# Kernel optimization log

Measured on AMD Instinct MI355X. Metric: run time of the kernel, lower is better.

## Reference

```python
import jax, jax.numpy as jnp
import numpy as np

NUM_HEADS = 4
C_IN = 80   # in_channels[0] (raw camera BEV channels)
C = 126     # in_channels[1]
D = C + 2   # 128, inner attention dim


def _conv(x, w, b=None):
    # NCHW conv, 3x3, SAME padding (padding=1)
    y = jax.lax.conv_general_dilated(x, w, (1, 1), 'SAME',
                                     dimension_numbers=('NCHW', 'OIHW', 'NCHW'))
    if b is not None:
        y = y + b[None, :, None, None]
    return y


def setup_inputs() -> dict:
    key = jax.random.key(0)
    ks = jax.random.split(key, 16)
    s = 0.02
    inp = {
        'lidar_bev': jax.random.normal(ks[0], (1, C, 64, 64), jnp.float32),
        'cam_bev': jax.random.normal(ks[1], (1, C_IN, 64, 64), jnp.float32),
        'cam_enc_w': jax.random.normal(ks[2], (C, C_IN, 3, 3), jnp.float32) * s,
        'cam_enc_b': jnp.zeros((C,), jnp.float32),
        'cam_v_w': jax.random.normal(ks[3], (D, C), jnp.float32) * s,
        'cam_qk_w': jax.random.normal(ks[4], (2 * D, C), jnp.float32) * s,
        'cam_proj_w': jax.random.normal(ks[5], (C, D), jnp.float32) * s,
        'cam_proj_b': jnp.zeros((C,), jnp.float32),
        'lidar_v_w': jax.random.normal(ks[6], (D, C), jnp.float32) * s,
        'lidar_qk_w': jax.random.normal(ks[7], (2 * D, C), jnp.float32) * s,
        'lidar_proj_w': jax.random.normal(ks[8], (C, D), jnp.float32) * s,
        'lidar_proj_b': jnp.zeros((C,), jnp.float32),
        'fuser_w': jax.random.normal(ks[9], (C, 4 * C, 3, 3), jnp.float32) * s,
    }
    return inp


def reference(lidar_bev, cam_bev, cam_enc_w, cam_enc_b, cam_v_w, cam_qk_w,
              cam_proj_w, cam_proj_b, lidar_v_w, lidar_qk_w, lidar_proj_w,
              lidar_proj_b, fuser_w):
    B, Cc, H, W = lidar_bev.shape
    N = H * W
    nh, hd = NUM_HEADS, D // NUM_HEADS
    scale = Cc ** (-0.5)  # in_channels[1] ** -0.5

    cam_enc = _conv(cam_bev, cam_enc_w, cam_enc_b)  # [B,C,H,W] (SCNET stand-in)

    cam_f = cam_enc.reshape(B, Cc, N).transpose(0, 2, 1)     # [B,N,C]
    lid_f = lidar_bev.reshape(B, Cc, N).transpose(0, 2, 1)    # [B,N,C]

    def heads(x):  # [B,N,D] -> [B,nh,N,hd]
        return x.reshape(B, N, nh, hd).transpose(0, 2, 1, 3)

    cam_v = heads(cam_f @ cam_v_w.T)
    lid_v = heads(lid_f @ lidar_v_w.T)

    def qk(x, w):  # -> (q, k) each [B,nh,N,hd]
        t = (x @ w.T).reshape(B, N, 2, nh, hd).transpose(2, 0, 3, 1, 4)
        return t[0], t[1]

    lid_q, lid_k = qk(lid_f, lidar_qk_w)
    cam_q, cam_k = qk(cam_f, cam_qk_w)

    def merge(o):  # [B,nh,N,hd] -> [B,N,D]
        return o.transpose(0, 2, 1, 3).reshape(B, N, D)

    def to_map(x):  # [B,N,C] -> [B,C,H,W]
        return x.reshape(B, H, W, Cc).transpose(0, 3, 1, 2)

    # lidar-driven attention, reused against two value tensors
    lid_attn = jax.nn.softmax(jnp.einsum('bhnd,bhmd->bhnm', lid_q, lid_k) * scale, axis=-1)
    cam_by_lid = to_map(merge(lid_attn @ cam_v) @ cam_proj_w.T + cam_proj_b)
    cam_bev_l = cam_enc + cam_by_lid
    lid_by_lid = to_map(merge(lid_attn @ lid_v) @ lidar_proj_w.T + lidar_proj_b)
    lidar_bev_l = lidar_bev + lid_by_lid

    # camera-driven attention (note: original code uses lidar_proj for BOTH outputs here)
    cam_attn = jax.nn.softmax(jnp.einsum('bhnd,bhmd->bhnm', cam_q, cam_k) * scale, axis=-1)
    cam_by_cam = to_map(merge(cam_attn @ cam_v) @ lidar_proj_w.T + lidar_proj_b)
    cam_bev_c = cam_enc + cam_by_cam
    lid_by_cam = to_map(merge(cam_attn @ lid_v) @ lidar_proj_w.T + lidar_proj_b)
    lidar_bev_c = lidar_bev + lid_by_cam

    fused_in = jnp.concatenate([cam_bev_c, cam_bev_l, lidar_bev_c, lidar_bev_l], axis=1)
    return _conv(fused_in, fuser_w)
```

## Files before the change

### kernel.cpp

```cpp
#include <hip/hip_runtime.h>
#include <hip/hip_bf16.h>

typedef unsigned short ushort_t;
using f32x4  = __attribute__((ext_vector_type(4))) float;
using f32x16 = __attribute__((ext_vector_type(16))) float;
using bf16x8 = __attribute__((ext_vector_type(8))) short;
typedef unsigned uint2v __attribute__((ext_vector_type(2)));

#define N_PIX 4096

static __device__ __forceinline__ unsigned short f2bf(float f) {
  unsigned int u = __builtin_bit_cast(unsigned int, f);
  u += 0x7FFFu + ((u >> 16) & 1u);
  return (unsigned short)(u >> 16);
}
static __device__ __forceinline__ float bf2f(unsigned int us) {
  return __builtin_bit_cast(float, us << 16);
}

typedef union {
  uint4 u4;
  unsigned u[4];
  unsigned long long q[2];
  bf16x8 v;
  unsigned short us[8];
} fragU;

#define LDS_U32(p) ((unsigned)(uintptr_t)((__attribute__((address_space(3))) void*)(p)))

static __device__ __forceinline__ size_t op_off(int s) {
  return (s < 9) ? ((size_t)s << 20)
       : (s == 9)  ? (size_t)15728640u
       : (s == 10) ? (size_t)19456000u
       :             (size_t)21553152u;
}
#define ML_OFF 16777216u

__global__ __launch_bounds__(256) void zero_span_k(uint4* __restrict__ p, int n16) {
  int i = blockIdx.x * 256 + threadIdx.x;
  if (i < n16) p[i] = (uint4){0u, 0u, 0u, 0u};
}

__global__ __launch_bounds__(256) void pack_w_k(
    const float* __restrict__ cam_enc_w, const float* __restrict__ fuser_w,
    const float* __restrict__ lid_proj_w, const float* __restrict__ cam_proj_w,
    const float* __restrict__ lid_qk_w, const float* __restrict__ cam_qk_w,
    const float* __restrict__ cam_v_w, const float* __restrict__ lid_v_w,
    ushort_t* __restrict__ Wp_c, ushort_t* __restrict__ Wp_f,
    ushort_t* __restrict__ Wp_lid, ushort_t* __restrict__ Wp_cam,
    ushort_t* __restrict__ Wq) {
  const float QSCALE = 0.08908708063747479f * 1.4426950408889634f;
  int idx = blockIdx.x * 256 + threadIdx.x;
  if (idx < 110592) {
    int kk = idx / 12288, r = idx % 12288;
    int co = r / 96, ci = r % 96;
    float v = (co < 126 && ci < 80) ? cam_enc_w[(co * 80 + ci) * 9 + kk] : 0.f;
    Wp_c[idx] = f2bf(v);
  } else if (idx < 700416) {
    int j = idx - 110592;
    int kk = j / 65536, r = j % 65536;
    int co = r / 512, ci = r % 512;
    float v = (co < 126 && ci < 504) ? fuser_w[(co * 504 + ci) * 9 + kk] : 0.f;
    Wp_f[j] = f2bf(v);
  } else if (idx < 716800) {
    int j = idx - 700416;
    int co = j >> 7, k = j & 127;
    Wp_lid[j] = f2bf(co < 126 ? lid_proj_w[co * 128 + k] : 0.f);
  } else if (idx < 733184) {
    int j = idx - 716800;
    int co = j >> 7, k = j & 127;
    Wp_cam[j] = f2bf(co < 126 ? cam_proj_w[co * 128 + k] : 0.f);
  } else if (idx < 831488) {
    int j = idx - 733184;
    int t = j >> 14, r = j & 16383;
    int row = r >> 7, ci = r & 127;
    float v = 0.f;
    if (ci < 126) {
      if (t == 0)      v = lid_qk_w[row * 126 + ci] * QSCALE;
      else if (t == 1) v = lid_qk_w[(128 + row) * 126 + ci];
      else if (t == 2) v = cam_qk_w[row * 126 + ci] * QSCALE;
      else if (t == 3) v = cam_qk_w[(128 + row) * 126 + ci];
      else if (t == 4) v = cam_v_w[row * 126 + ci];
      else             v = lid_v_w[row * 126 + ci];
    }
    Wq[j] = f2bf(v);
  }
}

__global__ __launch_bounds__(256) void convert_in_k(
    const float* __restrict__ cam, const float* __restrict__ lidar,
    ushort_t* __restrict__ m, ushort_t* __restrict__ h,
    ushort_t* __restrict__ lidBF) {
  int idx = blockIdx.x * 256 + threadIdx.x;
  if (idx < 327680) {
    int ch = idx >> 12, n = idx & 4095;
    int y = n >> 6, x = n & 63;
    unsigned short b = f2bf(cam[idx]);
    m[ch * 4224 + (y + 1) * 64 + x] = b;
    h[ch * 4356 + (y + 1) * 66 + (x + 1)] = b;
  } else {
    int j = idx - 327680;
    if (j < 516096) lidBF[j] = f2bf(lidar[j]);
  }
}

__global__ __launch_bounds__(256) void conv_mfma_k(
    const ushort_t* __restrict__ Amain,
    const ushort_t* __restrict__ Ahalo,
    const ushort_t* __restrict__ Wp,
    ushort_t* __restrict__ parts,
    int CIp, int ksteps) {
  __shared__ __align__(16) ushort_t Abuf[2][2048];
  const int y   = blockIdx.x;
  const int kk  = blockIdx.y;
  const int ky  = kk / 3, kx = kk - ky * 3;
  const int tid = threadIdx.x;
  const int w   = tid >> 6, l = tid & 63;
  const int lane15 = l & 15, g = l >> 4;
  const int yy1 = y + ky;

  const int ci_l = w * 8 + (l >> 5) * 4 + ((l & 7) >> 1);
  const int m0   = ((l >> 3) & 3) * 16 + (l & 1) * 8;
  const ushort_t* src;
  size_t plane;
  if (kx == 1) { plane = 66 * 64; src = Amain + (size_t)ci_l * plane + yy1 * 64 + m0; }
  else         { plane = 66 * 66; src = Ahalo + (size_t)ci_l * plane + yy1 * 66 + m0 + kx; }

  const ushort_t* wbase = Wp + ((size_t)kk * 128 + w * 32 + lane15) * CIp + g * 8;
  const unsigned tr_base = LDS_U32(&Abuf[0][0]) + (unsigned)(g * 1024 + lane15 * 8);

  f32x4 acc[4][2];
  #pragma unroll
  for (int q = 0; q < 4; ++q) {
    acc[q][0] = (f32x4){0.f, 0.f, 0.f, 0.f};
    acc[q][1] = (f32x4){0.f, 0.f, 0.f, 0.f};
  }

  __builtin_amdgcn_global_load_lds(
      (const __attribute__((address_space(1))) unsigned*)src,
      (__attribute__((address_space(3))) unsigned*)(&Abuf[0][w * 512]), 16, 0, 0);
  __syncthreads();

  for (int s = 0; s < ksteps; ++s) {
    if (s + 1 < ksteps) {
      const ushort_t* srcn = src + (size_t)(s + 1) * 32 * plane;
      __builtin_amdgcn_global_load_lds(
          (const __attribute__((address_space(1))) unsigned*)srcn,
          (__attribute__((address_space(3))) unsigned*)(&Abuf[(s + 1) & 1][w * 512]), 16, 0, 0);
    }
    const ushort_t* wb = wbase + s * 32;
    fragU fb0, fb1;
    fb0.u4 = *(const uint4*)(wb);
    fb1.u4 = *(const uint4*)(wb + 16 * CIp);

    unsigned ta = tr_base + (unsigned)((s & 1) << 12);
    unsigned long long r00, r01, r10, r11, r20, r21, r30, r31;
    asm volatile("ds_read_b64_tr_b16 %0, %1 offset:0"   : "=v"(r00) : "v"(ta));
    asm volatile("ds_read_b64_tr_b16 %0, %1 offset:512" : "=v"(r01) : "v"(ta));
    asm volatile("ds_read_b64_tr_b16 %0, %1 offset:128" : "=v"(r10) : "v"(ta));
    asm volatile("ds_read_b64_tr_b16 %0, %1 offset:640" : "=v"(r11) : "v"(ta));
    asm volatile("ds_read_b64_tr_b16 %0, %1 offset:256" : "=v"(r20) : "v"(ta));
    asm volatile("ds_read_b64_tr_b16 %0, %1 offset:768" : "=v"(r21) : "v"(ta));
    asm volatile("ds_read_b64_tr_b16 %0, %1 offset:384" : "=v"(r30) : "v"(ta));
    asm volatile("ds_read_b64_tr_b16 %0, %1 offset:896" : "=v"(r31) : "v"(ta));
    asm volatile("s_waitcnt lgkmcnt(0)" ::: "memory");
    __builtin_amdgcn_sched_barrier(0);

    fragU fa;
    fa.q[0] = r00; fa.q[1] = r01;
    acc[0][0] = __builtin_amdgcn_mfma_f32_16x16x32_bf16(fa.v, fb0.v, acc[0][0], 0, 0, 0);
    acc[0][1] = __builtin_amdgcn_mfma_f32_16x16x32_bf16(fa.v, fb1.v, acc[0][1], 0, 0, 0);
    fa.q[0] = r10; fa.q[1] = r11;
    acc[1][0] = __builtin_amdgcn_mfma_f32_16x16x32_bf16(fa.v, fb0.v, acc[1][0], 0, 0, 0);
    acc[1][1] = __builtin_amdgcn_mfma_f32_16x16x32_bf16(fa.v, fb1.v, acc[1][1], 0, 0, 0);
    fa.q[0] = r20; fa.q[1] = r21;
    acc[2][0] = __builtin_amdgcn_mfma_f32_16x16x32_bf16(fa.v, fb0.v, acc[2][0], 0, 0, 0);
    acc[2][1] = __builtin_amdgcn_mfma_f32_16x16x32_bf16(fa.v, fb1.v, acc[2][1], 0, 0, 0);
    fa.q[0] = r30; fa.q[1] = r31;
    acc[3][0] = __builtin_amdgcn_mfma_f32_16x16x32_bf16(fa.v, fb0.v, acc[3][0], 0, 0, 0);
    acc[3][1] = __builtin_amdgcn_mfma_f32_16x16x32_bf16(fa.v, fb1.v, acc[3][1], 0, 0, 0);
    __syncthreads();
  }

  ushort_t* pout = parts + (size_t)kk * 524288 + (size_t)(w * 32 + lane15) * 4096
                 + y * 64 + g * 4;
  #pragma unroll
  for (int q = 0; q < 4; ++q) {
    ushort4 p0, p1;
    p0.x = f2bf(acc[q][0][0]); p0.y = f2bf(acc[q][0][1]);
    p0.z = f2bf(acc[q][0][2]); p0.w = f2bf(acc[q][0][3]);
    p1.x = f2bf(acc[q][1][0]); p1.y = f2bf(acc[q][1][1]);
    p1.z = f2bf(acc[q][1][2]); p1.w = f2bf(acc[q][1][3]);
    *(ushort4*)(pout + q * 16)             = p0;
    *(ushort4*)(pout + 16 * 4096 + q * 16) = p1;
  }
}

__global__ __launch_bounds__(256) void reduce9_k(
    const ushort_t* __restrict__ parts, float* __restrict__ out,
    ushort_t* __restrict__ outbf, const float* __restrict__ bias) {
  int n0 = (blockIdx.x * 256 + threadIdx.x) * 8;
  int co = blockIdx.y;
  size_t off = (size_t)co * 4096 + n0;
  float s[8] = {0, 0, 0, 0, 0, 0, 0, 0};
  #pragma unroll
  for (int kk = 0; kk < 9; ++kk) {
    uint4 v = *(const uint4*)(parts + (size_t)kk * 524288 + off);
    s[0] += bf2f(v.x & 0xffffu); s[1] += bf2f(v.x >> 16);
    s[2] += bf2f(v.y & 0xffffu); s[3] += bf2f(v.y >> 16);
    s[4] += bf2f(v.z & 0xffffu); s[5] += bf2f(v.z >> 16);
    s[6] += bf2f(v.w & 0xffffu); s[7] += bf2f(v.w >> 16);
  }
  float b = bias ? bias[co] : 0.f;
  #pragma unroll
  for (int i = 0; i < 8; ++i) s[i] += b;
  if (out) {
    f32x4 o0 = {s[0], s[1], s[2], s[3]};
    f32x4 o1 = {s[4], s[5], s[6], s[7]};
    *(f32x4*)(out + off)     = o0;
    *(f32x4*)(out + off + 4) = o1;
  }
  if (outbf) {
    ushort4 b0, b1;
    b0.x = f2bf(s[0]); b0.y = f2bf(s[1]); b0.z = f2bf(s[2]); b0.w = f2bf(s[3]);
    b1.x = f2bf(s[4]); b1.y = f2bf(s[5]); b1.z = f2bf(s[6]); b1.w = f2bf(s[7]);
    *(ushort4*)(outbf + off)     = b0;
    *(ushort4*)(outbf + off + 4) = b1;
  }
}

__global__ __launch_bounds__(256) void qkv_mfma_k(
    const ushort_t* __restrict__ lidBF, const ushort_t* __restrict__ camBF,
    const ushort_t* __restrict__ Wq,
    ushort_t* __restrict__ lidQK, ushort_t* __restrict__ camQK,
    ushort_t* __restrict__ camV, ushort_t* __restrict__ lidV) {
  __shared__ __align__(16) ushort_t Abuf[2][2048];
  const int y = blockIdx.x, t = blockIdx.y;
  const ushort_t* X = (t >= 2 && t <= 4) ? camBF : lidBF;
  const int tid = threadIdx.x;
  const int w = tid >> 6, l = tid & 63;
  const int lane15 = l & 15, g = l >> 4;
  const int ci_l = w * 8 + (l >> 5) * 4 + ((l & 7) >> 1);
  const int m0   = ((l >> 3) & 3) * 16 + (l & 1) * 8;
  const ushort_t* src = X + (size_t)ci_l * 4096 + y * 64 + m0;
  const ushort_t* wbase = Wq + (size_t)t * 16384 + (w * 32 + lane15) * 128 + g * 8;
  const unsigned tr_base = LDS_U32(&Abuf[0][0]) + (unsigned)(g * 1024 + lane15 * 8);

  f32x4 acc[4][2];
  #pragma unroll
  for (int q = 0; q < 4; ++q) {
    acc[q][0] = (f32x4){0.f, 0.f, 0.f, 0.f};
    acc[q][1] = (f32x4){0.f, 0.f, 0.f, 0.f};
  }

  __builtin_amdgcn_global_load_lds(
      (const __attribute__((address_space(1))) unsigned*)src,
      (__attribute__((address_space(3))) unsigned*)(&Abuf[0][w * 512]), 16, 0, 0);
  __syncthreads();

  for (int s = 0; s < 4; ++s) {
    if (s < 3) {
      const ushort_t* srcn = src + (size_t)(s + 1) * 32 * 4096;
      __builtin_amdgcn_global_load_lds(
          (const __attribute__((address_space(1))) unsigned*)srcn,
          (__attribute__((address_space(3))) unsigned*)(&Abuf[(s + 1) & 1][w * 512]), 16, 0, 0);
    }
    const ushort_t* wb = wbase + s * 32;
    fragU fb0, fb1;
    fb0.u4 = *(const uint4*)(wb);
    fb1.u4 = *(const uint4*)(wb + 16 * 128);

    unsigned ta = tr_base + (unsigned)((s & 1) << 12);
    unsigned long long r00, r01, r10, r11, r20, r21, r30, r31;
    asm volatile("ds_read_b64_tr_b16 %0, %1 offset:0"   : "=v"(r00) : "v"(ta));
    asm volatile("ds_read_b64_tr_b16 %0, %1 offset:512" : "=v"(r01) : "v"(ta));
    asm volatile("ds_read_b64_tr_b16 %0, %1 offset:128" : "=v"(r10) : "v"(ta));
    asm volatile("ds_read_b64_tr_b16 %0, %1 offset:640" : "=v"(r11) : "v"(ta));
    asm volatile("ds_read_b64_tr_b16 %0, %1 offset:256" : "=v"(r20) : "v"(ta));
    asm volatile("ds_read_b64_tr_b16 %0, %1 offset:768" : "=v"(r21) : "v"(ta));
    asm volatile("ds_read_b64_tr_b16 %0, %1 offset:384" : "=v"(r30) : "v"(ta));
    asm volatile("ds_read_b64_tr_b16 %0, %1 offset:896" : "=v"(r31) : "v"(ta));
    asm volatile("s_waitcnt lgkmcnt(0)" ::: "memory");
    __builtin_amdgcn_sched_barrier(0);

    fragU fa;
    fa.q[0] = r00; fa.q[1] = r01;
    acc[0][0] = __builtin_amdgcn_mfma_f32_16x16x32_bf16(fa.v, fb0.v, acc[0][0], 0, 0, 0);
    acc[0][1] = __builtin_amdgcn_mfma_f32_16x16x32_bf16(fa.v, fb1.v, acc[0][1], 0, 0, 0);
    fa.q[0] = r10; fa.q[1] = r11;
    acc[1][0] = __builtin_amdgcn_mfma_f32_16x16x32_bf16(fa.v, fb0.v, acc[1][0], 0, 0, 0);
    acc[1][1] = __builtin_amdgcn_mfma_f32_16x16x32_bf16(fa.v, fb1.v, acc[1][1], 0, 0, 0);
    fa.q[0] = r20; fa.q[1] = r21;
    acc[2][0] = __builtin_amdgcn_mfma_f32_16x16x32_bf16(fa.v, fb0.v, acc[2][0], 0, 0, 0);
    acc[2][1] = __builtin_amdgcn_mfma_f32_16x16x32_bf16(fa.v, fb1.v, acc[2][1], 0, 0, 0);
    fa.q[0] = r30; fa.q[1] = r31;
    acc[3][0] = __builtin_amdgcn_mfma_f32_16x16x32_bf16(fa.v, fb0.v, acc[3][0], 0, 0, 0);
    acc[3][1] = __builtin_amdgcn_mfma_f32_16x16x32_bf16(fa.v, fb1.v, acc[3][1], 0, 0, 0);
    __syncthreads();
  }

  if (t < 4) {
    ushort_t* dst = (t < 2) ? lidQK : camQK;
    const int colbase = (t & 1) * 128 + w * 32 + lane15;
    #pragma unroll
    for (int q = 0; q < 4; ++q)
      #pragma unroll
      for (int tt = 0; tt < 2; ++tt)
        #pragma unroll
        for (int r = 0; r < 4; ++r) {
          int n = y * 64 + q * 16 + g * 4 + r;
          dst[(size_t)n * 256 + colbase + tt * 16] = f2bf(acc[q][tt][r]);
        }
  } else {
    ushort_t* dst = (t == 4) ? camV : lidV;
    ushort_t* pout = dst + (size_t)(w * 32 + lane15) * 4096 + y * 64 + g * 4;
    #pragma unroll
    for (int q = 0; q < 4; ++q) {
      ushort4 p0, p1;
      p0.x = f2bf(acc[q][0][0]); p0.y = f2bf(acc[q][0][1]);
      p0.z = f2bf(acc[q][0][2]); p0.w = f2bf(acc[q][0][3]);
      p1.x = f2bf(acc[q][1][0]); p1.y = f2bf(acc[q][1][1]);
      p1.z = f2bf(acc[q][1][2]); p1.w = f2bf(acc[q][1][3]);
      *(ushort4*)(pout + q * 16)             = p0;
      *(ushort4*)(pout + 16 * 4096 + q * 16) = p1;
    }
  }
}

__global__ __launch_bounds__(256) void flash_attn_mfma(
    const ushort_t* __restrict__ lidQK, const ushort_t* __restrict__ camQK,
    const ushort_t* __restrict__ camV, const ushort_t* __restrict__ lidV,
    char* __restrict__ ws) {
  const int i0    = blockIdx.x * 128;
  const int h     = blockIdx.y;
  const int z     = blockIdx.z;
  const int attn  = (z >= 3) ? 1 : 0;
  const int third = z - attn * 3;
  const int kbase = (third == 0) ? 0 : (1408 + (third - 1) * 1344);
  const int iters = (third == 0) ? 22 : 21;
  const ushort_t* QK = attn ? camQK : lidQK;

  __shared__ __align__(16) ushort_t Ks[2][64 * 40];
  __shared__ __align__(16) ushort_t Vt[2][64 * 72];

  const int tid = threadIdx.x;
  const int w = tid >> 6, l = tid & 63;
  const int q31 = l & 31, hi = l >> 5;
  const int q0w = i0 + w * 32;

  const int srow = tid >> 2, sc = tid & 3;
  const ushort_t* Kg = QK + (size_t)(kbase + srow) * 256 + 128 + h * 32 + sc * 8;
  const ushort_t* Vg = ((srow >> 5) ? lidV : camV)
                     + (size_t)(h * 32 + (srow & 31)) * N_PIX + kbase;

  fragU qf0, qf1;
  qf0.u4 = *(const uint4*)(QK + (size_t)(q0w + q31) * 256 + h * 32 + hi * 8);
  qf1.u4 = *(const uint4*)(QK + (size_t)(q0w + q31) * 256 + h * 32 + 16 + hi * 8);

  {
    uint4 k4 = *(const uint4*)Kg;
    uint4 va = *(const uint4*)(Vg + sc * 8);
    uint4 vb = *(const uint4*)(Vg + (sc + 4) * 8);
    *(uint4*)(&Ks[0][srow * 40 + sc * 8]) = k4;
    *(uint4*)(&Vt[0][srow * 72 + sc * 8]) = va;
    *(uint4*)(&Vt[0][srow * 72 + (sc + 4) * 8]) = vb;
  }
  __syncthreads();

  f32x16 Oc = (f32x16)0.f, Ol = (f32x16)0.f;
  float lrun = 0.f, mrun = -1e30f;

  for (int it = 0; it < iters; ++it) {
    const int cur = it & 1, nxt = cur ^ 1;
    const bool more = (it + 1) < iters;
    uint4 kn, van, vbn;
    if (more) {
      kn  = *(const uint4*)(Kg + (size_t)(it + 1) * 16384);
      van = *(const uint4*)(Vg + (it + 1) * 64 + sc * 8);
      vbn = *(const uint4*)(Vg + (it + 1) * 64 + (sc + 4) * 8);
    }

    const ushort_t* kb = &Ks[cur][0];
    fragU k00, k01, k10, k11;
    k00.u4 = *(const uint4*)(kb + q31 * 40 + hi * 8);
    k01.u4 = *(const uint4*)(kb + q31 * 40 + 16 + hi * 8);
    k10.u4 = *(const uint4*)(kb + (32 + q31) * 40 + hi * 8);
    k11.u4 = *(const uint4*)(kb + (32 + q31) * 40 + 16 + hi * 8);
    f32x16 S0, S1;
    __builtin_amdgcn_s_setprio(1);
    S0 = __builtin_amdgcn_mfma_f32_32x32x16_bf16(k00.v, qf0.v, (f32x16)0.f, 0, 0, 0);
    S0 = __builtin_amdgcn_mfma_f32_32x32x16_bf16(k01.v, qf1.v, S0, 0, 0, 0);
    S1 = __builtin_amdgcn_mfma_f32_32x32x16_bf16(k10.v, qf0.v, (f32x16)0.f, 0, 0, 0);
    S1 = __builtin_amdgcn_mfma_f32_32x32x16_bf16(k11.v, qf1.v, S1, 0, 0, 0);
    __builtin_amdgcn_s_setprio(0);

    float mx = S0[0];
    #pragma unroll
    for (int j = 1; j < 16; ++j) mx = fmaxf(mx, S0[j]);
    #pragma unroll
    for (int j = 0; j < 16; ++j) mx = fmaxf(mx, S1[j]);
    if (__any(mx > mrun + 6.f)) {
      float gm = mx;
      gm = fmaxf(gm, __shfl_xor(gm, 1));
      gm = fmaxf(gm, __shfl_xor(gm, 2));
      gm = fmaxf(gm, __shfl_xor(gm, 4));
      gm = fmaxf(gm, __shfl_xor(gm, 8));
      gm = fmaxf(gm, __shfl_xor(gm, 16));
      gm = fmaxf(gm, __shfl_xor(gm, 32));
      if (gm > mrun) {
        float corr = __builtin_amdgcn_exp2f(mrun - gm);
        Oc = Oc * corr;
        Ol = Ol * corr;
        lrun *= corr;
        mrun = gm;
      }
    }
    float ps = 0.f;
    #pragma unroll
    for (int j = 0; j < 16; ++j) {
      float p = __builtin_amdgcn_exp2f(S0[j] - mrun);
      S0[j] = p; ps += p;
    }
    #pragma unroll
    for (int j = 0; j < 16; ++j) {
      float p = __builtin_amdgcn_exp2f(S1[j] - mrun);
      S1[j] = p; ps += p;
    }
    ps += __shfl_xor(ps, 32);
    lrun += ps;

    fragU pa0, pa1, pa2, pa3;
    {
      unsigned a0, a1, b0, b1;
      asm("v_cvt_pk_bf16_f32 %0, %1, %2" : "=v"(a0) : "v"(S0[0]),  "v"(S0[1]));
      asm("v_cvt_pk_bf16_f32 %0, %1, %2" : "=v"(a1) : "v"(S0[2]),  "v"(S0[3]));
      asm("v_cvt_pk_bf16_f32 %0, %1, %2" : "=v"(b0) : "v"(S0[4]),  "v"(S0[5]));
      asm("v_cvt_pk_bf16_f32 %0, %1, %2" : "=v"(b1) : "v"(S0[6]),  "v"(S0[7]));
      uint2v r0 = __builtin_amdgcn_permlane32_swap(a0, b0, false, false);
      uint2v r1 = __builtin_amdgcn_permlane32_swap(a1, b1, false, false);
      pa0.u[0] = r0[0]; pa0.u[1] = r1[0]; pa0.u[2] = r0[1]; pa0.u[3] = r1[1];
      asm("v_cvt_pk_bf16_f32 %0, %1, %2" : "=v"(a0) : "v"(S0[8]),  "v"(S0[9]));
      asm("v_cvt_pk_bf16_f32 %0, %1, %2" : "=v"(a1) : "v"(S0[10]), "v"(S0[11]));
      asm("v_cvt_pk_bf16_f32 %0, %1, %2" : "=v"(b0) : "v"(S0[12]), "v"(S0[13]));
      asm("v_cvt_pk_bf16_f32 %0, %1, %2" : "=v"(b1) : "v"(S0[14]), "v"(S0[15]));
      r0 = __builtin_amdgcn_permlane32_swap(a0, b0, false, false);
      r1 = __builtin_amdgcn_permlane32_swap(a1, b1, false, false);
      pa1.u[0] = r0[0]; pa1.u[1] = r1[0]; pa1.u[2] = r0[1]; pa1.u[3] = r1[1];
      asm("v_cvt_pk_bf16_f32 %0, %1, %2" : "=v"(a0) : "v"(S1[0]),  "v"(S1[1]));
      asm("v_cvt_pk_bf16_f32 %0, %1, %2" : "=v"(a1) : "v"(S1[2]),  "v"(S1[3]));
      asm("v_cvt_pk_bf16_f32 %0, %1, %2" : "=v"(b0) : "v"(S1[4]),  "v"(S1[5]));
      asm("v_cvt_pk_bf16_f32 %0, %1, %2" : "=v"(b1) : "v"(S1[6]),  "v"(S1[7]));
      r0 = __builtin_amdgcn_permlane32_swap(a0, b0, false, false);
      r1 = __builtin_amdgcn_permlane32_swap(a1, b1, false, false);
      pa2.u[0] = r0[0]; pa2.u[1] = r1[0]; pa2.u[2] = r0[1]; pa2.u[3] = r1[1];
      asm("v_cvt_pk_bf16_f32 %0, %1, %2" : "=v"(a0) : "v"(S1[8]),  "v"(S1[9]));
      asm("v_cvt_pk_bf16_f32 %0, %1, %2" : "=v"(a1) : "v"(S1[10]), "v"(S1[11]));
      asm("v_cvt_pk_bf16_f32 %0, %1, %2" : "=v"(b0) : "v"(S1[12]), "v"(S1[13]));
      asm("v_cvt_pk_bf16_f32 %0, %1, %2" : "=v"(b1) : "v"(S1[14]), "v"(S1[15]));
      r0 = __builtin_amdgcn_permlane32_swap(a0, b0, false, false);
      r1 = __builtin_amdgcn_permlane32_swap(a1, b1, false, false);
      pa3.u[0] = r0[0]; pa3.u[1] = r1[0]; pa3.u[2] = r0[1]; pa3.u[3] = r1[1];
    }

    const ushort_t* vb = &Vt[cur][0];
    __builtin_amdgcn_s_setprio(1);
    {
      fragU vc, vl;
      vc.u4 = *(const uint4*)(vb + q31 * 72 + hi * 8);
      vl.u4 = *(const uint4*)(vb + (32 + q31) * 72 + hi * 8);
      Oc = __builtin_amdgcn_mfma_f32_32x32x16_bf16(pa0.v, vc.v, Oc, 0, 0, 0);
      Ol = __builtin_amdgcn_mfma_f32_32x32x16_bf16(pa0.v, vl.v, Ol, 0, 0, 0);
      vc.u4 = *(const uint4*)(vb + q31 * 72 + 16 + hi * 8);
      vl.u4 = *(const uint4*)(vb + (32 + q31) * 72 + 16 + hi * 8);
      Oc = __builtin_amdgcn_mfma_f32_32x32x16_bf16(pa1.v, vc.v, Oc, 0, 0, 0);
      Ol = __builtin_amdgcn_mfma_f32_32x32x16_bf16(pa1.v, vl.v, Ol, 0, 0, 0);
      vc.u4 = *(const uint4*)(vb + q31 * 72 + 32 + hi * 8);
      vl.u4 = *(const uint4*)(vb + (32 + q31) * 72 + 32 + hi * 8);
      Oc = __builtin_amdgcn_mfma_f32_32x32x16_bf16(pa2.v, vc.v, Oc, 0, 0, 0);
      Ol = __builtin_amdgcn_mfma_f32_32x32x16_bf16(pa2.v, vl.v, Ol, 0, 0, 0);
      vc.u4 = *(const uint4*)(vb + q31 * 72 + 48 + hi * 8);
      vl.u4 = *(const uint4*)(vb + (32 + q31) * 72 + 48 + hi * 8);
      Oc = __builtin_amdgcn_mfma_f32_32x32x16_bf16(pa3.v, vc.v, Oc, 0, 0, 0);
      Ol = __builtin_amdgcn_mfma_f32_32x32x16_bf16(pa3.v, vl.v, Ol, 0, 0, 0);
    }
    __builtin_amdgcn_s_setprio(0);

    if (more) {
      *(uint4*)(&Ks[nxt][srow * 40 + sc * 8]) = kn;
      *(uint4*)(&Vt[nxt][srow * 72 + sc * 8]) = van;
      *(uint4*)(&Vt[nxt][srow * 72 + (sc + 4) * 8]) = vbn;
    }
    __syncthreads();
  }

  const int si = (attn * 3 + third) * 2;
  ushort_t* OPc = (ushort_t*)(ws + op_off(si + 0));
  ushort_t* OPl = (ushort_t*)(ws + op_off(si + 1));
  float2* ML = (float2*)(ws + ML_OFF);
  const int d = h * 32 + q31;
  #pragma unroll
  for (int reg = 0; reg < 16; ++reg) {
    int n = q0w + (reg & 3) + 8 * (reg >> 2) + 4 * hi;
    OPc[(size_t)n * 128 + d] = f2bf(Oc[reg]);
    OPl[(size_t)n * 128 + d] = f2bf(Ol[reg]);
  }
  if (l < 32) {
    float2 v; v.x = mrun; v.y = lrun;
    ML[(size_t)(attn * 3 + third) * 4096 + q0w + l] = v;
  }
}

__global__ __launch_bounds__(256) void proj_mfma_k(
    const char* __restrict__ ws,
    const ushort_t* __restrict__ Wlid, const ushort_t* __restrict__ Wcam,
    const ushort_t* __restrict__ camBF, const float* __restrict__ lidar_bev,
    const float* __restrict__ cam_proj_b, const float* __restrict__ lid_proj_b,
    ushort_t* __restrict__ fm, ushort_t* __restrict__ fh) {
  const int n0 = blockIdx.x * 64;
  const int ot = blockIdx.y;
  const int attn = (ot == 0 || ot == 2) ? 1 : 0;
  const int vt = ot >> 1;
  const int tid = threadIdx.x;
  const int w = tid >> 6, l = tid & 63;
  const int m = l & 15, g = l >> 4;

  const float2* ML = (const float2*)(ws + ML_OFF);
  const int arow = n0 + w * 16 + m;

  float2 ml0 = ML[(size_t)(attn * 3 + 0) * 4096 + arow];
  float2 ml1 = ML[(size_t)(attn * 3 + 1) * 4096 + arow];
  float2 ml2 = ML[(size_t)(attn * 3 + 2) * 4096 + arow];
  float M = fmaxf(fmaxf(ml0.x, ml1.x), ml2.x);
  float w0 = __builtin_amdgcn_exp2f(ml0.x - M);
  float w1 = __builtin_amdgcn_exp2f(ml1.x - M);
  float w2 = __builtin_amdgcn_exp2f(ml2.x - M);
  float dn = w0 * ml0.y + w1 * ml1.y + w2 * ml2.y;
  float a0 = w0 / dn, a1 = w1 / dn, a2 = w2 / dn;

  const ushort_t* O0 = (const ushort_t*)(ws + op_off((attn * 3 + 0) * 2 + vt));
  const ushort_t* O1 = (const ushort_t*)(ws + op_off((attn * 3 + 1) * 2 + vt));
  const ushort_t* O2 = (const ushort_t*)(ws + op_off((attn * 3 + 2) * 2 + vt));

  fragU afr[4];
  #pragma unroll
  for (int s = 0; s < 4; ++s) {
    fragU x0, x1, x2;
    x0.u4 = *(const uint4*)(O0 + (size_t)arow * 128 + s * 32 + g * 8);
    x1.u4 = *(const uint4*)(O1 + (size_t)arow * 128 + s * 32 + g * 8);
    x2.u4 = *(const uint4*)(O2 + (size_t)arow * 128 + s * 32 + g * 8);
    #pragma unroll
    for (int j = 0; j < 8; ++j)
      afr[s].us[j] = f2bf(a0 * bf2f(x0.us[j]) + a1 * bf2f(x1.us[j])
                        + a2 * bf2f(x2.us[j]));
  }

  const ushort_t* W = (ot == 1) ? Wcam : Wlid;
  f32x4 acc[8];
  #pragma unroll
  for (int t = 0; t < 8; ++t) acc[t] = (f32x4){0.f, 0.f, 0.f, 0.f};
  #pragma unroll
  for (int s = 0; s < 4; ++s) {
    #pragma unroll
    for (int t = 0; t < 8; ++t) {
      fragU bfr;
      bfr.u4 = *(const uint4*)(W + (size_t)(t * 16 + m) * 128 + s * 32 + g * 8);
      acc[t] = __builtin_amdgcn_mfma_f32_16x16x32_bf16(afr[s].v, bfr.v, acc[t], 0, 0, 0);
    }
  }

  const float* bias = (ot == 1) ? cam_proj_b : lid_proj_b;
  const int doff = ot * 126;
  #pragma unroll
  for (int t = 0; t < 8; ++t) {
    int co = t * 16 + m;
    if (co < 126) {
      float b = bias[co];
      #pragma unroll
      for (int r = 0; r < 4; ++r) {
        int n = n0 + w * 16 + g * 4 + r;
        float res = (ot < 2) ? bf2f(camBF[(size_t)co * N_PIX + n])
                             : lidar_bev[(size_t)co * N_PIX + n];
        float v = acc[t][r] + res + b;
        unsigned short bf = f2bf(v);
        int y = n >> 6, x = n & 63;
        fm[(doff + co) * 4224 + (y + 1) * 64 + x]      = bf;
        fh[(doff + co) * 4356 + (y + 1) * 66 + x + 1]  = bf;
      }
    }
  }
}

extern "C" void kernel_launch(void* const* d_in, const int* in_sizes, int n_in,
                              void* d_out, int out_size, void* d_ws, size_t ws_size,
                              hipStream_t stream) {
  (void)in_sizes; (void)n_in; (void)out_size; (void)ws_size;
  const float* lidar_bev  = (const float*)d_in[0];
  const float* cam_bev    = (const float*)d_in[1];
  const float* cam_enc_w  = (const float*)d_in[2];
  const float* cam_enc_b  = (const float*)d_in[3];
  const float* cam_v_w    = (const float*)d_in[4];
  const float* cam_qk_w   = (const float*)d_in[5];
  const float* cam_proj_w = (const float*)d_in[6];
  const float* cam_proj_b = (const float*)d_in[7];
  const float* lid_v_w    = (const float*)d_in[8];
  const float* lid_qk_w   = (const float*)d_in[9];
  const float* lid_proj_w = (const float*)d_in[10];
  const float* lid_proj_b = (const float*)d_in[11];
  const float* fuser_w    = (const float*)d_in[12];
  float* out = (float*)d_out;

  char* p = (char*)d_ws;
  ushort_t* arena = (ushort_t*)p;
  ushort_t* lidQK = (ushort_t*)(p + 9437184);
  ushort_t* camQK = (ushort_t*)(p + 11534336);
  ushort_t* camV  = (ushort_t*)(p + 13631488);
  ushort_t* lidV  = (ushort_t*)(p + 14680064);
  ushort_t* Wp_c    = (ushort_t*)(p + 17793024);
  ushort_t* Wp_f    = (ushort_t*)(p + 18014208);
  ushort_t* Wp_lid  = (ushort_t*)(p + 19193856);
  ushort_t* Wp_cam  = (ushort_t*)(p + 19226624);
  ushort_t* Wq      = (ushort_t*)(p + 19259392);
  ushort_t* lidBF   = (ushort_t*)(p + 19456000);
  ushort_t* camBF   = (ushort_t*)(p + 20504576);
  ushort_t* camBF_m = (ushort_t*)(p + 21553152);
  ushort_t* camBF_h = (ushort_t*)(p + 22364160);
  ushort_t* fusBF_m = (ushort_t*)(p + 23200512);
  ushort_t* fusBF_h = (ushort_t*)(p + 27525888);

  zero_span_k<<<2548, 256, 0, stream>>>((uint4*)(p + 21553152), 652080);
  pack_w_k<<<3248, 256, 0, stream>>>(cam_enc_w, fuser_w, lid_proj_w, cam_proj_w,
                                     lid_qk_w, cam_qk_w, cam_v_w, lid_v_w,
                                     Wp_c, Wp_f, Wp_lid, Wp_cam, Wq);
  convert_in_k<<<3296, 256, 0, stream>>>(cam_bev, lidar_bev, camBF_m, camBF_h, lidBF);

  conv_mfma_k<<<dim3(64, 9), 256, 0, stream>>>(camBF_m, camBF_h, Wp_c, arena, 96, 3);
  reduce9_k<<<dim3(2, 126), 256, 0, stream>>>(arena, nullptr, camBF, cam_enc_b);

  qkv_mfma_k<<<dim3(64, 6), 256, 0, stream>>>(lidBF, camBF, Wq, lidQK, camQK, camV, lidV);
  flash_attn_mfma<<<dim3(32, 4, 6), 256, 0, stream>>>(lidQK, camQK, camV, lidV, p);
  proj_mfma_k<<<dim3(64, 4), 256, 0, stream>>>(p, Wp_lid, Wp_cam, camBF, lidar_bev,
                                               cam_proj_b, lid_proj_b, fusBF_m, fusBF_h);

  conv_mfma_k<<<dim3(64, 9), 256, 0, stream>>>(fusBF_m, fusBF_h, Wp_f, arena, 512, 16);
  reduce9_k<<<dim3(2, 126), 256, 0, stream>>>(arena, out, nullptr, nullptr);
}
```

Measured before the change: 119.8 us.

## Load flash-attention K/V fragments directly from global and merge prep kernels

The flash attention kernel drops its double-buffered LDS staging of K and V tiles and the per-iteration block barrier. Each wave now loads its MFMA operand fragments straight from global memory (relying on L2/L1 for reuse across the four waves). Separately, the weight-packing and input-conversion kernels are merged into one launch to save a kernel launch. The risk is redundant global traffic and exposed load latency without the software prefetch.

```diff
diff --git a/kernel.cpp b/kernel.cpp
--- a/kernel.cpp
+++ b/kernel.cpp
@@ -41,14 +41,17 @@
   if (i < n16) p[i] = (uint4){0u, 0u, 0u, 0u};
 }
 
-__global__ __launch_bounds__(256) void pack_w_k(
+__global__ __launch_bounds__(256) void prep_k(
     const float* __restrict__ cam_enc_w, const float* __restrict__ fuser_w,
     const float* __restrict__ lid_proj_w, const float* __restrict__ cam_proj_w,
     const float* __restrict__ lid_qk_w, const float* __restrict__ cam_qk_w,
     const float* __restrict__ cam_v_w, const float* __restrict__ lid_v_w,
+    const float* __restrict__ cam_bev, const float* __restrict__ lidar_bev,
     ushort_t* __restrict__ Wp_c, ushort_t* __restrict__ Wp_f,
     ushort_t* __restrict__ Wp_lid, ushort_t* __restrict__ Wp_cam,
-    ushort_t* __restrict__ Wq) {
+    ushort_t* __restrict__ Wq,
+    ushort_t* __restrict__ cm, ushort_t* __restrict__ ch_,
+    ushort_t* __restrict__ lidBF) {
   const float QSCALE = 0.08908708063747479f * 1.4426950408889634f;
   int idx = blockIdx.x * 256 + threadIdx.x;
   if (idx < 110592) {
@@ -84,23 +87,18 @@
       else             v = lid_v_w[row * 126 + ci];
     }
     Wq[j] = f2bf(v);
-  }
-}
-
-__global__ __launch_bounds__(256) void convert_in_k(
-    const float* __restrict__ cam, const float* __restrict__ lidar,
-    ushort_t* __restrict__ m, ushort_t* __restrict__ h,
-    ushort_t* __restrict__ lidBF) {
-  int idx = blockIdx.x * 256 + threadIdx.x;
-  if (idx < 327680) {
-    int ch = idx >> 12, n = idx & 4095;
-    int y = n >> 6, x = n & 63;
-    unsigned short b = f2bf(cam[idx]);
-    m[ch * 4224 + (y + 1) * 64 + x] = b;
-    h[ch * 4356 + (y + 1) * 66 + (x + 1)] = b;
   } else {
-    int j = idx - 327680;
-    if (j < 516096) lidBF[j] = f2bf(lidar[j]);
+    int k = idx - 831488;
+    if (k < 327680) {
+      int ch = k >> 12, n = k & 4095;
+      int y = n >> 6, x = n & 63;
+      unsigned short b = f2bf(cam_bev[k]);
+      cm[ch * 4224 + (y + 1) * 64 + x] = b;
+      ch_[ch * 4356 + (y + 1) * 66 + (x + 1)] = b;
+    } else {
+      int j = k - 327680;
+      if (j < 516096) lidBF[j] = f2bf(lidar_bev[j]);
+    }
   }
 }
 
@@ -340,52 +338,41 @@
   const int iters = (third == 0) ? 22 : 21;
   const ushort_t* QK = attn ? camQK : lidQK;
 
-  __shared__ __align__(16) ushort_t Ks[2][64 * 40];
-  __shared__ __align__(16) ushort_t Vt[2][64 * 72];
-
   const int tid = threadIdx.x;
   const int w = tid >> 6, l = tid & 63;
   const int q31 = l & 31, hi = l >> 5;
   const int q0w = i0 + w * 32;
 
-  const int srow = tid >> 2, sc = tid & 3;
-  const ushort_t* Kg = QK + (size_t)(kbase + srow) * 256 + 128 + h * 32 + sc * 8;
-  const ushort_t* Vg = ((srow >> 5) ? lidV : camV)
-                     + (size_t)(h * 32 + (srow & 31)) * N_PIX + kbase;
-
   fragU qf0, qf1;
   qf0.u4 = *(const uint4*)(QK + (size_t)(q0w + q31) * 256 + h * 32 + hi * 8);
   qf1.u4 = *(const uint4*)(QK + (size_t)(q0w + q31) * 256 + h * 32 + 16 + hi * 8);
 
-  {
-    uint4 k4 = *(const uint4*)Kg;
-    uint4 va = *(const uint4*)(Vg + sc * 8);
-    uint4 vb = *(const uint4*)(Vg + (sc + 4) * 8);
-    *(uint4*)(&Ks[0][srow * 40 + sc * 8]) = k4;
-    *(uint4*)(&Vt[0][srow * 72 + sc * 8]) = va;
-    *(uint4*)(&Vt[0][srow * 72 + (sc + 4) * 8]) = vb;
-  }
-  __syncthreads();
+  const ushort_t* Kp = QK + (size_t)(kbase + q31) * 256 + 128 + h * 32 + hi * 8;
+  const ushort_t* Vc = camV + (size_t)(h * 32 + q31) * N_PIX + kbase + hi * 8;
+  const ushort_t* Vl = lidV + (size_t)(h * 32 + q31) * N_PIX + kbase + hi * 8;
 
   f32x16 Oc = (f32x16)0.f, Ol = (f32x16)0.f;
   float lrun = 0.f, mrun = -1e30f;
 
   for (int it = 0; it < iters; ++it) {
-    const int cur = it & 1, nxt = cur ^ 1;
-    const bool more = (it + 1) < iters;
-    uint4 kn, van, vbn;
-    if (more) {
-      kn  = *(const uint4*)(Kg + (size_t)(it + 1) * 16384);
-      van = *(const uint4*)(Vg + (it + 1) * 64 + sc * 8);
-      vbn = *(const uint4*)(Vg + (it + 1) * 64 + (sc + 4) * 8);
-    }
-
-    const ushort_t* kb = &Ks[cur][0];
     fragU k00, k01, k10, k11;
-    k00.u4 = *(const uint4*)(kb + q31 * 40 + hi * 8);
-    k01.u4 = *(const uint4*)(kb + q31 * 40 + 16 + hi * 8);
-    k10.u4 = *(const uint4*)(kb + (32 + q31) * 40 + hi * 8);
-    k11.u4 = *(const uint4*)(kb + (32 + q31) * 40 + 16 + hi * 8);
+    const ushort_t* kp = Kp + (size_t)it * 16384;
+    k00.u4 = *(const uint4*)(kp);
+    k01.u4 = *(const uint4*)(kp + 16);
+    k10.u4 = *(const uint4*)(kp + 8192);
+    k11.u4 = *(const uint4*)(kp + 8192 + 16);
+    fragU vc0, vc1, vc2, vc3, vl0, vl1, vl2, vl3;
+    const ushort_t* vcp = Vc + it * 64;
+    const ushort_t* vlp = Vl + it * 64;
+    vc0.u4 = *(const uint4*)(vcp);
+    vc1.u4 = *(const uint4*)(vcp + 16);
+    vc2.u4 = *(const uint4*)(vcp + 32);
+    vc3.u4 = *(const uint4*)(vcp + 48);
+    vl0.u4 = *(const uint4*)(vlp);
+    vl1.u4 = *(const uint4*)(vlp + 16);
+    vl2.u4 = *(const uint4*)(vlp + 32);
+    vl3.u4 = *(const uint4*)(vlp + 48);
+
     f32x16 S0, S1;
     __builtin_amdgcn_s_setprio(1);
     S0 = __builtin_amdgcn_mfma_f32_32x32x16_bf16(k00.v, qf0.v, (f32x16)0.f, 0, 0, 0);
@@ -462,35 +449,16 @@
       pa3.u[0] = r0[0]; pa3.u[1] = r1[0]; pa3.u[2] = r0[1]; pa3.u[3] = r1[1];
     }
 
-    const ushort_t* vb = &Vt[cur][0];
     __builtin_amdgcn_s_setprio(1);
-    {
-      fragU vc, vl;
-      vc.u4 = *(const uint4*)(vb + q31 * 72 + hi * 8);
-      vl.u4 = *(const uint4*)(vb + (32 + q31) * 72 + hi * 8);
-      Oc = __builtin_amdgcn_mfma_f32_32x32x16_bf16(pa0.v, vc.v, Oc, 0, 0, 0);
-      Ol = __builtin_amdgcn_mfma_f32_32x32x16_bf16(pa0.v, vl.v, Ol, 0, 0, 0);
-      vc.u4 = *(const uint4*)(vb + q31 * 72 + 16 + hi * 8);
-      vl.u4 = *(const uint4*)(vb + (32 + q31) * 72 + 16 + hi * 8);
-      Oc = __builtin_amdgcn_mfma_f32_32x32x16_bf16(pa1.v, vc.v, Oc, 0, 0, 0);
-      Ol = __builtin_amdgcn_mfma_f32_32x32x16_bf16(pa1.v, vl.v, Ol, 0, 0, 0);
-      vc.u4 = *(const uint4*)(vb + q31 * 72 + 32 + hi * 8);
-      vl.u4 = *(const uint4*)(vb + (32 + q31) * 72 + 32 + hi * 8);
-      Oc = __builtin_amdgcn_mfma_f32_32x32x16_bf16(pa2.v, vc.v, Oc, 0, 0, 0);
-      Ol = __builtin_amdgcn_mfma_f32_32x32x16_bf16(pa2.v, vl.v, Ol, 0, 0, 0);
-      vc.u4 = *(const uint4*)(vb + q31 * 72 + 48 + hi * 8);
-      vl.u4 = *(const uint4*)(vb + (32 + q31) * 72 + 48 + hi * 8);
-      Oc = __builtin_amdgcn_mfma_f32_32x32x16_bf16(pa3.v, vc.v, Oc, 0, 0, 0);
-      Ol = __builtin_amdgcn_mfma_f32_32x32x16_bf16(pa3.v, vl.v, Ol, 0, 0, 0);
-    }
+    Oc = __builtin_amdgcn_mfma_f32_32x32x16_bf16(pa0.v, vc0.v, Oc, 0, 0, 0);
+    Ol = __builtin_amdgcn_mfma_f32_32x32x16_bf16(pa0.v, vl0.v, Ol, 0, 0, 0);
+    Oc = __builtin_amdgcn_mfma_f32_32x32x16_bf16(pa1.v, vc1.v, Oc, 0, 0, 0);
+    Ol = __builtin_amdgcn_mfma_f32_32x32x16_bf16(pa1.v, vl1.v, Ol, 0, 0, 0);
+    Oc = __builtin_amdgcn_mfma_f32_32x32x16_bf16(pa2.v, vc2.v, Oc, 0, 0, 0);
+    Ol = __builtin_amdgcn_mfma_f32_32x32x16_bf16(pa2.v, vl2.v, Ol, 0, 0, 0);
+    Oc = __builtin_amdgcn_mfma_f32_32x32x16_bf16(pa3.v, vc3.v, Oc, 0, 0, 0);
+    Ol = __builtin_amdgcn_mfma_f32_32x32x16_bf16(pa3.v, vl3.v, Ol, 0, 0, 0);
     __builtin_amdgcn_s_setprio(0);
-
-    if (more) {
-      *(uint4*)(&Ks[nxt][srow * 40 + sc * 8]) = kn;
-      *(uint4*)(&Vt[nxt][srow * 72 + sc * 8]) = van;
-      *(uint4*)(&Vt[nxt][srow * 72 + (sc + 4) * 8]) = vbn;
-    }
-    __syncthreads();
   }
 
   const int si = (attn * 3 + third) * 2;
@@ -628,10 +596,11 @@
   ushort_t* fusBF_h = (ushort_t*)(p + 27525888);
 
   zero_span_k<<<2548, 256, 0, stream>>>((uint4*)(p + 21553152), 652080);
-  pack_w_k<<<3248, 256, 0, stream>>>(cam_enc_w, fuser_w, lid_proj_w, cam_proj_w,
-                                     lid_qk_w, cam_qk_w, cam_v_w, lid_v_w,
-                                     Wp_c, Wp_f, Wp_lid, Wp_cam, Wq);
-  convert_in_k<<<3296, 256, 0, stream>>>(cam_bev, lidar_bev, camBF_m, camBF_h, lidBF);
+  prep_k<<<6544, 256, 0, stream>>>(cam_enc_w, fuser_w, lid_proj_w, cam_proj_w,
+                                   lid_qk_w, cam_qk_w, cam_v_w, lid_v_w,
+                                   cam_bev, lidar_bev,
+                                   Wp_c, Wp_f, Wp_lid, Wp_cam, Wq,
+                                   camBF_m, camBF_h, lidBF);
 
   conv_mfma_k<<<dim3(64, 9), 256, 0, stream>>>(camBF_m, camBF_h, Wp_c, arena, 96, 3);
   reduce9_k<<<dim3(2, 126), 256, 0, stream>>>(arena, nullptr, camBF, cam_enc_b);
```

Result: slower. 166.0 us (+38.5%).
